# Performance work log

Hardware: AMD Instinct MI355X
Metric: run time of the kernel (lower is better)

## Reference

```python
import jax, jax.numpy as jnp
import numpy as np
import math

B, H, S, D = 2, 16, 2048, 64

def setup_inputs() -> dict:
    key = jax.random.key(0)
    kq, kk, kv = jax.random.split(key, 3)
    Q = jax.random.normal(kq, (B, H, S, D), dtype=jnp.float32)
    K = jax.random.normal(kk, (B, H, S, D), dtype=jnp.float32)
    V = jax.random.normal(kv, (B, H, S, D), dtype=jnp.float32)
    # causal mask, broadcastable over batch and heads; 0 -> masked out
    mask = jnp.tril(jnp.ones((S, S), dtype=jnp.int32))[None, None, :, :]
    return {"Q": Q, "K": K, "V": V, "mask": mask}

def reference(Q, K, V, mask):
    d_k = Q.shape[-1]
    # scores: [B, H, S, S]
    scores = jnp.einsum("bhqd,bhkd->bhqk", Q, K) / math.sqrt(d_k)
    scores = jnp.where(mask == 0, jnp.float32(-1e9), scores)
    attn_weights = jax.nn.softmax(scores, axis=-1)
    output = jnp.einsum("bhqk,bhkd->bhqd", attn_weights, V)
    return (output, attn_weights)
```

## Files before the change

### kernel.cpp

```cpp
#include <hip/hip_runtime.h>
#include <hip/hip_bf16.h>


#define S_ 2048
#define D_ 64
#define BH_ 32

typedef short short8 __attribute__((ext_vector_type(8)));
typedef float f32x4 __attribute__((ext_vector_type(4)));
typedef unsigned short ushort4v __attribute__((ext_vector_type(4)));

__device__ __forceinline__ unsigned short f2bf(float f) {
  union { float f; unsigned u; } c; c.f = f;
  unsigned u = c.u + 0x7fffu + ((c.u >> 16) & 1u);
  return (unsigned short)(u >> 16);
}

__device__ __forceinline__ void g2l16(const void* g, void* l) {
  __builtin_amdgcn_global_load_lds(
      (const __attribute__((address_space(1))) unsigned int*)g,
      (__attribute__((address_space(3))) unsigned int*)l, 16, 0, 0);
}

__global__ __launch_bounds__(256) void cvt_bf16(const float* __restrict__ src,
                                                unsigned short* __restrict__ dst, int n4) {
  int i = blockIdx.x * 256 + threadIdx.x;
  if (i < n4) {
    float4 v = ((const float4*)src)[i];
    ushort4v u = { f2bf(v.x), f2bf(v.y), f2bf(v.z), f2bf(v.w) };
    ((ushort4v*)dst)[i] = u;
  }
}

__global__ __launch_bounds__(256) void vtrans(const float* __restrict__ V,
                                              unsigned short* __restrict__ Vt) {
  __shared__ float T[64][65];
  const int bh = blockIdx.x >> 5, st = blockIdx.x & 31;
  const int tid = threadIdx.x;
  const float* src = V + ((size_t)bh * S_ + st * 64) * D_;
  for (int i = tid; i < 1024; i += 256) {
    int e = i * 4; int r = e >> 6; int c = e & 63;
    float4 v = *(const float4*)(src + e);
    T[r][c] = v.x; T[r][c + 1] = v.y; T[r][c + 2] = v.z; T[r][c + 3] = v.w;
  }
  __syncthreads();
  const int d = tid >> 2;
  const int sc = (tid & 3) * 16;
  unsigned short* dst = Vt + ((size_t)bh * D_ + d) * S_ + st * 64 + sc;
#pragma unroll
  for (int j = 0; j < 16; ++j) dst[j] = f2bf(T[sc + j][d]);
}

__global__ __launch_bounds__(256, 4)
void sdpa_main(const unsigned short* __restrict__ Qg, const unsigned short* __restrict__ Kg,
               const unsigned short* __restrict__ Vtg, float* __restrict__ Og,
               float* __restrict__ Pg) {
  __shared__ __align__(16) unsigned short Qs[64 * 64];
  __shared__ __align__(16) unsigned short Kb2[2][64 * 64];
  __shared__ __align__(16) unsigned short Ps[64][72];

  const int tid = threadIdx.x;
  const int wave = tid >> 6;
  const int lane = tid & 63;
  const int m = lane & 15;
  const int quad = lane >> 4;

  const int bh = blockIdx.x & 31;
  const int qb = 31 - (blockIdx.x >> 5);
  const int q0 = qb * 64;
  const int ktiles = qb + 1;

  const unsigned short* Qb = Qg + ((size_t)bh * S_ + q0) * D_;
  const unsigned short* Kb = Kg + (size_t)bh * S_ * D_;
  const unsigned short* Vb = Vtg + (size_t)bh * D_ * S_;

  auto stageK = [&](const unsigned short* gbase, unsigned short* lbase) {
#pragma unroll
    for (int j = 0; j < 2; ++j) {
      int g = wave * 2 + j;
      int row = g * 8 + (lane >> 3);
      int c = (lane & 7) ^ (row & 7);
      g2l16(gbase + row * 64 + c * 8, lbase + g * 512);
    }
  };
  auto stageV = [&](int kt, unsigned short* lbase) {
#pragma unroll
    for (int j = 0; j < 2; ++j) {
      int g = wave * 2 + j;
      int d = g * 8 + (lane >> 3);
      int c = (lane & 7) ^ (d & 7);
      g2l16(Vb + (size_t)d * S_ + kt * 64 + c * 8, lbase + g * 512);
    }
  };
  auto frag = [&](const unsigned short* base, int row, int kc) -> short8 {
    int c = (kc * 4 + quad) ^ (row & 7);
    return *(const short8*)(base + row * 64 + c * 8);
  };

  stageK(Qb, Qs);
  stageK(Kb, Kb2[0]);
  {
    const int zc4 = (31 - qb) * 16;
    if (zc4 > 0) {
      float4 z = make_float4(0.f, 0.f, 0.f, 0.f);
      float* base = Pg + ((size_t)(bh * S_ + q0 + wave * 16)) * S_ + (q0 + 64);
#pragma unroll 1
      for (int r = 0; r < 16; ++r)
        for (int i = lane; i < zc4; i += 64)
          *(float4*)(base + (size_t)r * S_ + i * 4) = z;
    }
  }

  float lsum[4] = {0.f, 0.f, 0.f, 0.f};
  for (int kt = 0; kt < ktiles; ++kt) {
    __syncthreads();
    if (kt + 1 < ktiles) stageK(Kb + (kt + 1) * 64 * 64, Kb2[(kt + 1) & 1]);
    const unsigned short* Kt = Kb2[kt & 1];
    const bool diag = (kt == qb);
#pragma unroll
    for (int nt = 0; nt < 4; ++nt) {
      f32x4 acc = {0.f, 0.f, 0.f, 0.f};
#pragma unroll
      for (int kc = 0; kc < 2; ++kc)
        acc = __builtin_amdgcn_mfma_f32_16x16x32_bf16(
            frag(Qs, wave * 16 + m, kc), frag(Kt, nt * 16 + m, kc), acc, 0, 0, 0);
      if (diag) {
        const int kg = kt * 64 + nt * 16 + m;
#pragma unroll
        for (int r = 0; r < 4; ++r) {
          const int qg = q0 + wave * 16 + quad * 4 + r;
          lsum[r] += (kg > qg) ? 0.f : __expf(acc[r] * 0.125f);
        }
      } else {
#pragma unroll
        for (int r = 0; r < 4; ++r) lsum[r] += __expf(acc[r] * 0.125f);
      }
    }
  }

  float invl[4];
#pragma unroll
  for (int r = 0; r < 4; ++r) {
    float v = lsum[r];
    v += __shfl_xor(v, 1); v += __shfl_xor(v, 2);
    v += __shfl_xor(v, 4); v += __shfl_xor(v, 8);
    invl[r] = 1.0f / v;
  }

  f32x4 oacc[4];
#pragma unroll
  for (int dt = 0; dt < 4; ++dt) oacc[dt] = (f32x4){0.f, 0.f, 0.f, 0.f};

  for (int kt = 0; kt < ktiles; ++kt) {
    __syncthreads();
    stageK(Kb + kt * 64 * 64, Kb2[0]);
    stageV(kt, Kb2[1]);
    __syncthreads();
    const bool diag = (kt == qb);
#pragma unroll
    for (int nt = 0; nt < 4; ++nt) {
      f32x4 acc = {0.f, 0.f, 0.f, 0.f};
#pragma unroll
      for (int kc = 0; kc < 2; ++kc)
        acc = __builtin_amdgcn_mfma_f32_16x16x32_bf16(
            frag(Qs, wave * 16 + m, kc), frag(Kb2[0], nt * 16 + m, kc), acc, 0, 0, 0);
      const int kg = kt * 64 + nt * 16 + m;
#pragma unroll
      for (int r = 0; r < 4; ++r) {
        const int qg = q0 + wave * 16 + quad * 4 + r;
        float p = (diag && kg > qg) ? 0.f : __expf(acc[r] * 0.125f) * invl[r];
        Pg[(size_t)(bh * S_ + qg) * S_ + kg] = p;
        Ps[wave * 16 + quad * 4 + r][nt * 16 + m] = f2bf(p);
      }
    }
#pragma unroll
    for (int dt = 0; dt < 4; ++dt)
#pragma unroll
      for (int kc = 0; kc < 2; ++kc) {
        short8 a = *(const short8*)&Ps[wave * 16 + m][kc * 32 + quad * 8];
        short8 b = frag(Kb2[1], dt * 16 + m, kc);
        oacc[dt] = __builtin_amdgcn_mfma_f32_16x16x32_bf16(a, b, oacc[dt], 0, 0, 0);
      }
  }

#pragma unroll
  for (int dt = 0; dt < 4; ++dt)
#pragma unroll
    for (int r = 0; r < 4; ++r)
      Og[(size_t)(bh * S_ + q0 + wave * 16 + quad * 4 + r) * D_ + dt * 16 + m] =
          oacc[dt][r];
}

extern "C" void kernel_launch(void* const* d_in, const int* in_sizes, int n_in,
                              void* d_out, int out_size, void* d_ws, size_t ws_size,
                              hipStream_t stream) {
  const float* Q = (const float*)d_in[0];
  const float* K = (const float*)d_in[1];
  const float* V = (const float*)d_in[2];
  float* Og = (float*)d_out;
  float* Pg = (float*)d_out + (size_t)BH_ * S_ * D_;

  unsigned short* Qbf = (unsigned short*)d_ws;
  unsigned short* Kbf = Qbf + (size_t)BH_ * S_ * D_;
  unsigned short* Vt  = Kbf + (size_t)BH_ * S_ * D_;

  const int n4 = (BH_ * S_ * D_) / 4;
  cvt_bf16<<<dim3(n4 / 256), dim3(256), 0, stream>>>(Q, Qbf, n4);
  cvt_bf16<<<dim3(n4 / 256), dim3(256), 0, stream>>>(K, Kbf, n4);
  vtrans<<<dim3(1024), dim3(256), 0, stream>>>(V, Vt);
  sdpa_main<<<dim3(1024), dim3(256), 0, stream>>>(Qbf, Kbf, Vt, Og, Pg);
}
```

Before: 676.8 us.

## Load Q/K/V fragments straight to registers, drop LDS staging and barriers

Removes the LDS staging of Q, K and V along with the block-wide barriers. Each wave now loads its MFMA fragments directly from global memory into registers, using a software-pipelined double buffer for K. The block-to-query-tile mapping is reordered to balance the causal workload, the stores of P and of the zero fill become nontemporal, and the launch bound occupancy drops from 4 to 3. The direct loads are less coalesced and are repeated by every wave, and the extra fragment registers raise register pressure.

```diff
diff --git a/kernel.cpp b/kernel.cpp
--- a/kernel.cpp
+++ b/kernel.cpp
@@ -14,12 +14,6 @@
   union { float f; unsigned u; } c; c.f = f;
   unsigned u = c.u + 0x7fffu + ((c.u >> 16) & 1u);
   return (unsigned short)(u >> 16);
-}
-
-__device__ __forceinline__ void g2l16(const void* g, void* l) {
-  __builtin_amdgcn_global_load_lds(
-      (const __attribute__((address_space(1))) unsigned int*)g,
-      (__attribute__((address_space(3))) unsigned int*)l, 16, 0, 0);
 }
 
 __global__ __launch_bounds__(256) void cvt_bf16(const float* __restrict__ src,
@@ -51,12 +45,10 @@
   for (int j = 0; j < 16; ++j) dst[j] = f2bf(T[sc + j][d]);
 }
 
-__global__ __launch_bounds__(256, 4)
+__global__ __launch_bounds__(256, 3)
 void sdpa_main(const unsigned short* __restrict__ Qg, const unsigned short* __restrict__ Kg,
                const unsigned short* __restrict__ Vtg, float* __restrict__ Og,
                float* __restrict__ Pg) {
-  __shared__ __align__(16) unsigned short Qs[64 * 64];
-  __shared__ __align__(16) unsigned short Kb2[2][64 * 64];
   __shared__ __align__(16) unsigned short Ps[64][72];
 
   const int tid = threadIdx.x;
@@ -66,64 +58,48 @@
   const int quad = lane >> 4;
 
   const int bh = blockIdx.x & 31;
-  const int qb = 31 - (blockIdx.x >> 5);
+  const int t = blockIdx.x >> 5;
+  const int sg = t >> 3, g = t & 7;
+  const int qb = (sg == 0) ? 16 + g : (sg == 1) ? 31 - g : (sg == 2) ? 15 - g : g;
   const int q0 = qb * 64;
   const int ktiles = qb + 1;
 
-  const unsigned short* Qb = Qg + ((size_t)bh * S_ + q0) * D_;
-  const unsigned short* Kb = Kg + (size_t)bh * S_ * D_;
-  const unsigned short* Vb = Vtg + (size_t)bh * D_ * S_;
-
-  auto stageK = [&](const unsigned short* gbase, unsigned short* lbase) {
-#pragma unroll
-    for (int j = 0; j < 2; ++j) {
-      int g = wave * 2 + j;
-      int row = g * 8 + (lane >> 3);
-      int c = (lane & 7) ^ (row & 7);
-      g2l16(gbase + row * 64 + c * 8, lbase + g * 512);
-    }
-  };
-  auto stageV = [&](int kt, unsigned short* lbase) {
-#pragma unroll
-    for (int j = 0; j < 2; ++j) {
-      int g = wave * 2 + j;
-      int d = g * 8 + (lane >> 3);
-      int c = (lane & 7) ^ (d & 7);
-      g2l16(Vb + (size_t)d * S_ + kt * 64 + c * 8, lbase + g * 512);
-    }
-  };
-  auto frag = [&](const unsigned short* base, int row, int kc) -> short8 {
-    int c = (kc * 4 + quad) ^ (row & 7);
-    return *(const short8*)(base + row * 64 + c * 8);
-  };
-
-  stageK(Qb, Qs);
-  stageK(Kb, Kb2[0]);
+  const unsigned short* Kbh = Kg + (size_t)bh * S_ * D_;
+  const unsigned short* Vbh = Vtg + (size_t)bh * D_ * S_;
+
+  const unsigned short* Qrow = Qg + ((size_t)bh * S_ + q0 + wave * 16 + m) * D_;
+  const short8 qf0 = *(const short8*)(Qrow + quad * 8);
+  const short8 qf1 = *(const short8*)(Qrow + 32 + quad * 8);
+
   {
     const int zc4 = (31 - qb) * 16;
     if (zc4 > 0) {
-      float4 z = make_float4(0.f, 0.f, 0.f, 0.f);
+      f32x4 z = {0.f, 0.f, 0.f, 0.f};
       float* base = Pg + ((size_t)(bh * S_ + q0 + wave * 16)) * S_ + (q0 + 64);
 #pragma unroll 1
       for (int r = 0; r < 16; ++r)
         for (int i = lane; i < zc4; i += 64)
-          *(float4*)(base + (size_t)r * S_ + i * 4) = z;
-    }
-  }
+          __builtin_nontemporal_store(z, (f32x4*)(base + (size_t)r * S_ + i * 4));
+    }
+  }
+
+  auto loadK = [&](int kt, short8 (&kf)[4][2]) {
+    const unsigned short* kb = Kbh + (size_t)kt * 64 * 64;
+#pragma unroll
+    for (int nt = 0; nt < 4; ++nt)
+#pragma unroll
+      for (int kc = 0; kc < 2; ++kc)
+        kf[nt][kc] = *(const short8*)(kb + (nt * 16 + m) * 64 + (kc * 4 + quad) * 8);
+  };
 
   float lsum[4] = {0.f, 0.f, 0.f, 0.f};
-  for (int kt = 0; kt < ktiles; ++kt) {
-    __syncthreads();
-    if (kt + 1 < ktiles) stageK(Kb + (kt + 1) * 64 * 64, Kb2[(kt + 1) & 1]);
-    const unsigned short* Kt = Kb2[kt & 1];
+  auto procA = [&](int kt, const short8 (&kf)[4][2]) {
     const bool diag = (kt == qb);
 #pragma unroll
     for (int nt = 0; nt < 4; ++nt) {
       f32x4 acc = {0.f, 0.f, 0.f, 0.f};
-#pragma unroll
-      for (int kc = 0; kc < 2; ++kc)
-        acc = __builtin_amdgcn_mfma_f32_16x16x32_bf16(
-            frag(Qs, wave * 16 + m, kc), frag(Kt, nt * 16 + m, kc), acc, 0, 0, 0);
+      acc = __builtin_amdgcn_mfma_f32_16x16x32_bf16(qf0, kf[nt][0], acc, 0, 0, 0);
+      acc = __builtin_amdgcn_mfma_f32_16x16x32_bf16(qf1, kf[nt][1], acc, 0, 0, 0);
       if (diag) {
         const int kg = kt * 64 + nt * 16 + m;
 #pragma unroll
@@ -136,6 +112,19 @@
         for (int r = 0; r < 4; ++r) lsum[r] += __expf(acc[r] * 0.125f);
       }
     }
+  };
+
+  short8 kfA[4][2], kfB[4][2];
+  loadK(0, kfA);
+  for (int kt = 0; kt < ktiles; kt += 2) {
+    if (kt + 1 < ktiles) {
+      loadK(kt + 1, kfB);
+      procA(kt, kfA);
+      if (kt + 2 < ktiles) loadK(kt + 2, kfA);
+      procA(kt + 1, kfB);
+    } else {
+      procA(kt, kfA);
+    }
   }
 
   float invl[4];
@@ -151,36 +140,41 @@
 #pragma unroll
   for (int dt = 0; dt < 4; ++dt) oacc[dt] = (f32x4){0.f, 0.f, 0.f, 0.f};
 
+  loadK(0, kfA);
   for (int kt = 0; kt < ktiles; ++kt) {
-    __syncthreads();
-    stageK(Kb + kt * 64 * 64, Kb2[0]);
-    stageV(kt, Kb2[1]);
-    __syncthreads();
+    short8 vf[4][2];
+#pragma unroll
+    for (int dt = 0; dt < 4; ++dt)
+#pragma unroll
+      for (int kc = 0; kc < 2; ++kc)
+        vf[dt][kc] = *(const short8*)(Vbh + (size_t)(dt * 16 + m) * S_ +
+                                      kt * 64 + (kc * 4 + quad) * 8);
+
     const bool diag = (kt == qb);
 #pragma unroll
     for (int nt = 0; nt < 4; ++nt) {
       f32x4 acc = {0.f, 0.f, 0.f, 0.f};
-#pragma unroll
-      for (int kc = 0; kc < 2; ++kc)
-        acc = __builtin_amdgcn_mfma_f32_16x16x32_bf16(
-            frag(Qs, wave * 16 + m, kc), frag(Kb2[0], nt * 16 + m, kc), acc, 0, 0, 0);
+      acc = __builtin_amdgcn_mfma_f32_16x16x32_bf16(qf0, kfA[nt][0], acc, 0, 0, 0);
+      acc = __builtin_amdgcn_mfma_f32_16x16x32_bf16(qf1, kfA[nt][1], acc, 0, 0, 0);
       const int kg = kt * 64 + nt * 16 + m;
 #pragma unroll
       for (int r = 0; r < 4; ++r) {
         const int qg = q0 + wave * 16 + quad * 4 + r;
         float p = (diag && kg > qg) ? 0.f : __expf(acc[r] * 0.125f) * invl[r];
-        Pg[(size_t)(bh * S_ + qg) * S_ + kg] = p;
+        __builtin_nontemporal_store(p, Pg + (size_t)(bh * S_ + qg) * S_ + kg);
         Ps[wave * 16 + quad * 4 + r][nt * 16 + m] = f2bf(p);
       }
     }
-#pragma unroll
-    for (int dt = 0; dt < 4; ++dt)
-#pragma unroll
-      for (int kc = 0; kc < 2; ++kc) {
-        short8 a = *(const short8*)&Ps[wave * 16 + m][kc * 32 + quad * 8];
-        short8 b = frag(Kb2[1], dt * 16 + m, kc);
-        oacc[dt] = __builtin_amdgcn_mfma_f32_16x16x32_bf16(a, b, oacc[dt], 0, 0, 0);
-      }
+
+    if (kt + 1 < ktiles) loadK(kt + 1, kfA);
+
+    const short8 pa0 = *(const short8*)&Ps[wave * 16 + m][quad * 8];
+    const short8 pa1 = *(const short8*)&Ps[wave * 16 + m][32 + quad * 8];
+#pragma unroll
+    for (int dt = 0; dt < 4; ++dt) {
+      oacc[dt] = __builtin_amdgcn_mfma_f32_16x16x32_bf16(pa0, vf[dt][0], oacc[dt], 0, 0, 0);
+      oacc[dt] = __builtin_amdgcn_mfma_f32_16x16x32_bf16(pa1, vf[dt][1], oacc[dt], 0, 0, 0);
+    }
   }
 
 #pragma unroll
```

Result: slower. 720.5 us (+6.5%).

## Double-buffer K/V in second pass, keep Q in registers, nontemporal P stores

Applied to the files above, without the earlier changes.

The second pass now double-buffers both K and V tiles, prefetching tile kt+1 while computing tile kt, so one barrier per iteration is removed. Q fragments are loaded once into registers instead of staged through LDS. The attention-weight and zero-fill stores become nontemporal to reduce cache pollution, the P tile in LDS uses an XOR swizzle instead of padding, and the query-block-to-workgroup mapping is reordered to balance causal work. This adds LDS use (four K/V buffers) and register pressure, which may reduce occupancy. The ordering of the single barrier against the async global-to-LDS loads and the Ps writes and reads also looks fragile.

```diff
diff --git a/kernel.cpp b/kernel.cpp
--- a/kernel.cpp
+++ b/kernel.cpp
@@ -55,9 +55,9 @@
 void sdpa_main(const unsigned short* __restrict__ Qg, const unsigned short* __restrict__ Kg,
                const unsigned short* __restrict__ Vtg, float* __restrict__ Og,
                float* __restrict__ Pg) {
-  __shared__ __align__(16) unsigned short Qs[64 * 64];
   __shared__ __align__(16) unsigned short Kb2[2][64 * 64];
-  __shared__ __align__(16) unsigned short Ps[64][72];
+  __shared__ __align__(16) unsigned short Vb2[2][64 * 64];
+  __shared__ __align__(16) unsigned short Ps[64 * 64];
 
   const int tid = threadIdx.x;
   const int wave = tid >> 6;
@@ -66,30 +66,35 @@
   const int quad = lane >> 4;
 
   const int bh = blockIdx.x & 31;
-  const int qb = 31 - (blockIdx.x >> 5);
+  const int t = blockIdx.x >> 5;
+  const int sg = t >> 3, g = t & 7;
+  const int qb = (sg == 0) ? 16 + g : (sg == 1) ? 31 - g : (sg == 2) ? 15 - g : g;
   const int q0 = qb * 64;
   const int ktiles = qb + 1;
 
-  const unsigned short* Qb = Qg + ((size_t)bh * S_ + q0) * D_;
-  const unsigned short* Kb = Kg + (size_t)bh * S_ * D_;
-  const unsigned short* Vb = Vtg + (size_t)bh * D_ * S_;
+  const unsigned short* Kbh = Kg + (size_t)bh * S_ * D_;
+  const unsigned short* Vbh = Vtg + (size_t)bh * D_ * S_;
+
+  const unsigned short* Qrow = Qg + ((size_t)bh * S_ + q0 + wave * 16 + m) * D_;
+  const short8 qf0 = *(const short8*)(Qrow + quad * 8);
+  const short8 qf1 = *(const short8*)(Qrow + 32 + quad * 8);
 
   auto stageK = [&](const unsigned short* gbase, unsigned short* lbase) {
 #pragma unroll
     for (int j = 0; j < 2; ++j) {
-      int g = wave * 2 + j;
-      int row = g * 8 + (lane >> 3);
+      int gi = wave * 2 + j;
+      int row = gi * 8 + (lane >> 3);
       int c = (lane & 7) ^ (row & 7);
-      g2l16(gbase + row * 64 + c * 8, lbase + g * 512);
+      g2l16(gbase + row * 64 + c * 8, lbase + gi * 512);
     }
   };
   auto stageV = [&](int kt, unsigned short* lbase) {
 #pragma unroll
     for (int j = 0; j < 2; ++j) {
-      int g = wave * 2 + j;
-      int d = g * 8 + (lane >> 3);
+      int gi = wave * 2 + j;
+      int d = gi * 8 + (lane >> 3);
       int c = (lane & 7) ^ (d & 7);
-      g2l16(Vb + (size_t)d * S_ + kt * 64 + c * 8, lbase + g * 512);
+      g2l16(Vbh + (size_t)d * S_ + kt * 64 + c * 8, lbase + gi * 512);
     }
   };
   auto frag = [&](const unsigned short* base, int row, int kc) -> short8 {
@@ -97,33 +102,30 @@
     return *(const short8*)(base + row * 64 + c * 8);
   };
 
-  stageK(Qb, Qs);
-  stageK(Kb, Kb2[0]);
+  stageK(Kbh, Kb2[0]);
   {
     const int zc4 = (31 - qb) * 16;
     if (zc4 > 0) {
-      float4 z = make_float4(0.f, 0.f, 0.f, 0.f);
+      f32x4 z = {0.f, 0.f, 0.f, 0.f};
       float* base = Pg + ((size_t)(bh * S_ + q0 + wave * 16)) * S_ + (q0 + 64);
 #pragma unroll 1
       for (int r = 0; r < 16; ++r)
         for (int i = lane; i < zc4; i += 64)
-          *(float4*)(base + (size_t)r * S_ + i * 4) = z;
+          __builtin_nontemporal_store(z, (f32x4*)(base + (size_t)r * S_ + i * 4));
     }
   }
 
   float lsum[4] = {0.f, 0.f, 0.f, 0.f};
   for (int kt = 0; kt < ktiles; ++kt) {
     __syncthreads();
-    if (kt + 1 < ktiles) stageK(Kb + (kt + 1) * 64 * 64, Kb2[(kt + 1) & 1]);
+    if (kt + 1 < ktiles) stageK(Kbh + (kt + 1) * 64 * 64, Kb2[(kt + 1) & 1]);
     const unsigned short* Kt = Kb2[kt & 1];
     const bool diag = (kt == qb);
 #pragma unroll
     for (int nt = 0; nt < 4; ++nt) {
       f32x4 acc = {0.f, 0.f, 0.f, 0.f};
-#pragma unroll
-      for (int kc = 0; kc < 2; ++kc)
-        acc = __builtin_amdgcn_mfma_f32_16x16x32_bf16(
-            frag(Qs, wave * 16 + m, kc), frag(Kt, nt * 16 + m, kc), acc, 0, 0, 0);
+      acc = __builtin_amdgcn_mfma_f32_16x16x32_bf16(qf0, frag(Kt, nt * 16 + m, 0), acc, 0, 0, 0);
+      acc = __builtin_amdgcn_mfma_f32_16x16x32_bf16(qf1, frag(Kt, nt * 16 + m, 1), acc, 0, 0, 0);
       if (diag) {
         const int kg = kt * 64 + nt * 16 + m;
 #pragma unroll
@@ -138,6 +140,10 @@
     }
   }
 
+  __syncthreads();
+  stageK(Kbh, Kb2[0]);
+  stageV(0, Vb2[0]);
+
   float invl[4];
 #pragma unroll
   for (int r = 0; r < 4; ++r) {
@@ -153,32 +159,36 @@
 
   for (int kt = 0; kt < ktiles; ++kt) {
     __syncthreads();
-    stageK(Kb + kt * 64 * 64, Kb2[0]);
-    stageV(kt, Kb2[1]);
-    __syncthreads();
+    if (kt + 1 < ktiles) {
+      stageK(Kbh + (kt + 1) * 64 * 64, Kb2[(kt + 1) & 1]);
+      stageV(kt + 1, Vb2[(kt + 1) & 1]);
+    }
+    const unsigned short* Kt = Kb2[kt & 1];
+    const unsigned short* Vt = Vb2[kt & 1];
     const bool diag = (kt == qb);
 #pragma unroll
     for (int nt = 0; nt < 4; ++nt) {
       f32x4 acc = {0.f, 0.f, 0.f, 0.f};
-#pragma unroll
-      for (int kc = 0; kc < 2; ++kc)
-        acc = __builtin_amdgcn_mfma_f32_16x16x32_bf16(
-            frag(Qs, wave * 16 + m, kc), frag(Kb2[0], nt * 16 + m, kc), acc, 0, 0, 0);
+      acc = __builtin_amdgcn_mfma_f32_16x16x32_bf16(qf0, frag(Kt, nt * 16 + m, 0), acc, 0, 0, 0);
+      acc = __builtin_amdgcn_mfma_f32_16x16x32_bf16(qf1, frag(Kt, nt * 16 + m, 1), acc, 0, 0, 0);
       const int kg = kt * 64 + nt * 16 + m;
 #pragma unroll
       for (int r = 0; r < 4; ++r) {
         const int qg = q0 + wave * 16 + quad * 4 + r;
         float p = (diag && kg > qg) ? 0.f : __expf(acc[r] * 0.125f) * invl[r];
-        Pg[(size_t)(bh * S_ + qg) * S_ + kg] = p;
-        Ps[wave * 16 + quad * 4 + r][nt * 16 + m] = f2bf(p);
+        __builtin_nontemporal_store(p, Pg + (size_t)(bh * S_ + qg) * S_ + kg);
+        const int prow = wave * 16 + quad * 4 + r;
+        const int pcol = nt * 16 + m;
+        Ps[prow * 64 + (pcol & 7) + ((((pcol >> 3) ^ (prow & 7))) << 3)] = f2bf(p);
       }
     }
 #pragma unroll
     for (int dt = 0; dt < 4; ++dt)
 #pragma unroll
       for (int kc = 0; kc < 2; ++kc) {
-        short8 a = *(const short8*)&Ps[wave * 16 + m][kc * 32 + quad * 8];
-        short8 b = frag(Kb2[1], dt * 16 + m, kc);
+        const int prow = wave * 16 + m;
+        short8 a = *(const short8*)&Ps[prow * 64 + (((kc * 4 + quad) ^ (prow & 7)) << 3)];
+        short8 b = frag(Vt, dt * 16 + m, kc);
         oacc[dt] = __builtin_amdgcn_mfma_f32_16x16x32_bf16(a, b, oacc[dt], 0, 0, 0);
       }
   }
```

New measurement: 666.5 us. No clear change (-1.5%).
